# Optimization experiments

Hardware: AMD Instinct MI355X
Metric: run time of the kernel (lower is better)

The kernel has to match this reference:

```python
import jax, jax.numpy as jnp
import numpy as np

N_POINTS, D_EMBED, N_CLUSTERS = 131072, 512, 512
ALPHA = 100.0   # softmax sharpness (python scalar in original forward)
LAMBD = 0.1     # loss weight (init arg in original)


def setup_inputs() -> dict:
    key = jax.random.key(0)
    k1, k2 = jax.random.split(key)
    embeddings = jax.random.normal(k1, (N_POINTS, D_EMBED), dtype=jnp.float32)
    centroids = jax.random.normal(k2, (N_CLUSTERS, D_EMBED), dtype=jnp.float32)
    alpha = jnp.float32(ALPHA)
    lambd = jnp.float32(LAMBD)
    return {"embeddings": embeddings, "centroids": centroids, "alpha": alpha, "lambd": lambd}


def reference(embeddings, centroids, alpha, lambd):
    # Squared euclidean distance to every centroid, computed via GEMM expansion
    # instead of the original per-centroid python loop:
    #   dist[n, k] = ||x_n||^2 - 2 x_n . c_k + ||c_k||^2
    x2 = jnp.sum(embeddings * embeddings, axis=1, keepdims=True)   # [N, 1]
    c2 = jnp.sum(centroids * centroids, axis=1)                    # [K]
    dist = x2 - 2.0 * (embeddings @ centroids.T) + c2[None, :]     # [N, K]
    # Original: exp(-alpha*(d - min_k d)) / sum == stable softmax of -alpha*d over k.
    w = jax.nn.softmax(-alpha * dist, axis=1)                      # [N, K]
    # lambd * mean over points of softmax-weighted distance sum over clusters.
    return lambd * jnp.mean(jnp.sum(dist * w, axis=1))
```

## Files before the change

kernel.cpp:

```cpp
#include <hip/hip_runtime.h>
#include <stdint.h>

#define NPTS   131072
#define DEMB   512
#define NCL    512
#define BM     64
#define NCHUNK 8
#define NTHREADS 256
#define NBLK   (NPTS / BM)

typedef __attribute__((ext_vector_type(4))) float f32x4;

#define WS_CB   0u
#define WS_C2   262144u
#define WS_PART 264192u

static __device__ __forceinline__ float sq4(f32x4 v) {
  return v[0] * v[0] + v[1] * v[1] + v[2] * v[2] + v[3] * v[3];
}

#define LOAD_B8F(DST, BASE)                                                    \
  asm volatile("global_load_dwordx2 %0, %8, off\n\t"                           \
               "global_load_dwordx2 %1, %8, off offset:512\n\t"                \
               "global_load_dwordx2 %2, %8, off offset:1024\n\t"               \
               "global_load_dwordx2 %3, %8, off offset:1536\n\t"               \
               "global_load_dwordx2 %4, %8, off offset:2048\n\t"               \
               "global_load_dwordx2 %5, %8, off offset:2560\n\t"               \
               "global_load_dwordx2 %6, %8, off offset:3072\n\t"               \
               "global_load_dwordx2 %7, %8, off offset:3584"                   \
               : "=&v"((DST)[0]), "=&v"((DST)[1]), "=&v"((DST)[2]),            \
                 "=&v"((DST)[3]), "=&v"((DST)[4]), "=&v"((DST)[5]),            \
                 "=&v"((DST)[6]), "=&v"((DST)[7])                              \
               : "v"(BASE)                                                     \
               : "memory")

#define LOAD_E4(D, P)                                                          \
  asm volatile("global_load_dwordx4 %0, %4, off\n\t"                           \
               "global_load_dwordx4 %1, %4, off offset:16\n\t"                 \
               "global_load_dwordx4 %2, %4, off offset:32\n\t"                 \
               "global_load_dwordx4 %3, %4, off offset:48"                     \
               : "=&v"(D[0]), "=&v"(D[1]), "=&v"(D[2]), "=&v"(D[3])            \
               : "v"(P)                                                        \
               : "memory")

#define WAITV(N)                                                               \
  do {                                                                         \
    asm volatile("s_waitcnt vmcnt(" #N ")" ::: "memory");                      \
    __builtin_amdgcn_sched_barrier(0);                                         \
  } while (0)

#define BAR()                                                                  \
  do {                                                                         \
    asm volatile("s_waitcnt lgkmcnt(0)" ::: "memory");                         \
    __builtin_amdgcn_s_barrier();                                              \
  } while (0)

__global__ __launch_bounds__(128) void prep_kernel(const float* __restrict__ cent,
                                                   uint8_t* __restrict__ ws) {
  const int k = blockIdx.x;
  const int t = threadIdx.x;
  float4 v = ((const float4*)(cent + (size_t)k * DEMB))[t];
  float sq = v.x * v.x + v.y * v.y + v.z * v.z + v.w * v.w;
#pragma unroll
  for (int m = 1; m < 64; m <<= 1) sq += __shfl_xor(sq, m, 64);
  __shared__ float red[2];
  if ((t & 63) == 0) red[t >> 6] = sq;
  __syncthreads();
  if (t == 0) ((float*)(ws + WS_C2))[k] = red[0] + red[1];

  int p = __builtin_amdgcn_cvt_pk_fp8_f32(v.x, v.y, 0, false);
  p = __builtin_amdgcn_cvt_pk_fp8_f32(v.z, v.w, p, true);

  const int d = t * 4;
  const int ch = d >> 6;
  const int dd = d & 63;
  const int kk = dd >> 5;
  const int lhi = (dd >> 3) & 3;
  const int w = k >> 7;
  const int n = (k >> 4) & 7;
  const int l15 = k & 15;
  const int lane = lhi * 16 + l15;
  const uint32_t off = (uint32_t)(ch * 32768 + w * 8192 + kk * 4096 + n * 512 +
                                  lane * 8 + (dd & 7));
  *(uint32_t*)(ws + WS_CB + off) = (uint32_t)p;
}

__global__ __launch_bounds__(NTHREADS, 2) void main_kernel(
    const float* __restrict__ emb, const uint8_t* __restrict__ ws,
    const float* __restrict__ alphap) {
  __shared__ uint8_t Ab[2][4096];
  __shared__ float redmin[256];
  __shared__ float redse[256];
  __shared__ float redsge[256];
  __shared__ float gmin[64];
  __shared__ float x2s[64];

  const int t = threadIdx.x;
  const int w = t >> 6;
  const int l = t & 63;
  const int l15 = l & 15;
  const int lhi = l >> 4;
  const int bid = blockIdx.x;
  const size_t row0 = (size_t)bid * BM;

  float* partials = (float*)(ws + WS_PART);

  f32x4 acc[4][8];
#pragma unroll
  for (int m = 0; m < 4; ++m)
#pragma unroll
    for (int n = 0; n < 8; ++n) acc[m][n] = (f32x4){0.f, 0.f, 0.f, 0.f};

  const int r = t >> 2;
  const int q = t & 3;
  const float* xge = emb + (row0 + r) * DEMB + q * 16;
  uint32_t xoff[2];
#pragma unroll
  for (int j = 0; j < 2; ++j)
    xoff[j] = (uint32_t)r * 64u + (uint32_t)(((2 * q + j) ^ (r & 7)) << 3);

  float x2a = 0.f;

  const uint8_t* fbw = ws + WS_CB + (uint32_t)w * 8192u + (uint32_t)l * 8u;

  long bA[16], bB[16];
  f32x4 ev0[4], ev1[4];

#define STAGE_FROM(EV, DSTBUF)                                                 \
  do {                                                                         \
    uint8_t* _an = (DSTBUF);                                                   \
    _Pragma("unroll")                                                          \
    for (int j = 0; j < 2; ++j) {                                              \
      f32x4 a = EV[2 * j], b = EV[2 * j + 1];                                  \
      x2a += sq4(a) + sq4(b);                                                  \
      uint2 u;                                                                 \
      int p0 = __builtin_amdgcn_cvt_pk_fp8_f32(a[0], a[1], 0, false);          \
      p0 = __builtin_amdgcn_cvt_pk_fp8_f32(a[2], a[3], p0, true);              \
      int p1 = __builtin_amdgcn_cvt_pk_fp8_f32(b[0], b[1], 0, false);          \
      p1 = __builtin_amdgcn_cvt_pk_fp8_f32(b[2], b[3], p1, true);              \
      u.x = (uint32_t)p0;                                                      \
      u.y = (uint32_t)p1;                                                      \
      *(uint2*)(_an + xoff[j]) = u;                                            \
    }                                                                          \
  } while (0)

  LOAD_E4(ev0, xge);
  LOAD_E4(ev1, xge + 64);
  LOAD_B8F(&bA[0], fbw);
  LOAD_B8F(&bA[8], fbw + 4096);
  WAITV(20);
  STAGE_FROM(ev0, &Ab[0][0]);
  BAR();

#define CHUNK_BODY(CH, BCUR, BNEXT, EVN, EVS, VN)                              \
  {                                                                            \
    if ((CH) + 2 < NCHUNK)                                                     \
      LOAD_E4(EVN, xge + ((CH) + 2) * 64);                                     \
    if ((CH) + 1 < NCHUNK) {                                                   \
      const uint8_t* nb = fbw + (uint32_t)((CH) + 1) * 32768u;                 \
      LOAD_B8F(&BNEXT[0], nb);                                                 \
      LOAD_B8F(&BNEXT[8], nb + 4096);                                          \
    }                                                                          \
    const uint8_t* xb = &Ab[(CH) & 1][0];                                      \
    WAITV(VN);                                                                 \
    __builtin_amdgcn_s_setprio(1);                                             \
    _Pragma("unroll")                                                          \
    for (int kk = 0; kk < 2; ++kk) {                                           \
      const uint32_t swz = (uint32_t)(((kk * 4 + lhi) ^ (l15 & 7)) << 3);      \
      long af[4];                                                              \
      _Pragma("unroll")                                                        \
      for (int m = 0; m < 4; ++m)                                              \
        af[m] = *(const long*)(xb + (uint32_t)(m * 16 + l15) * 64u + swz);     \
      _Pragma("unroll")                                                        \
      for (int m = 0; m < 4; ++m)                                              \
        _Pragma("unroll")                                                      \
        for (int n = 0; n < 8; ++n)                                            \
          acc[m][n] = __builtin_amdgcn_mfma_f32_16x16x32_fp8_fp8(              \
              af[m], BCUR[kk * 8 + n], acc[m][n], 0, 0, 0);                    \
    }                                                                          \
    __builtin_amdgcn_s_setprio(0);                                             \
    if ((CH) + 1 < NCHUNK)                                                     \
      STAGE_FROM(EVS, &Ab[((CH) + 1) & 1][0]);                                 \
    BAR();                                                                     \
  }

  CHUNK_BODY(0, bA, bB, ev0, ev1, 20)
  CHUNK_BODY(1, bB, bA, ev1, ev0, 20)
  CHUNK_BODY(2, bA, bB, ev0, ev1, 20)
  CHUNK_BODY(3, bB, bA, ev1, ev0, 20)
  CHUNK_BODY(4, bA, bB, ev0, ev1, 20)
  CHUNK_BODY(5, bB, bA, ev1, ev0, 20)
  CHUNK_BODY(6, bA, bB, ev0, ev1, 16)
  CHUNK_BODY(7, bB, bA, ev1, ev0, 0)
#undef CHUNK_BODY
#undef STAGE_FROM

  const float alpha = alphap[0];
  float c2r[8];
  {
    const float* c2p = (const float*)(ws + WS_C2) + w * 128 + l15;
    asm volatile("global_load_dword %0, %8, off\n\t"
                 "global_load_dword %1, %8, off offset:64\n\t"
                 "global_load_dword %2, %8, off offset:128\n\t"
                 "global_load_dword %3, %8, off offset:192\n\t"
                 "global_load_dword %4, %8, off offset:256\n\t"
                 "global_load_dword %5, %8, off offset:320\n\t"
                 "global_load_dword %6, %8, off offset:384\n\t"
                 "global_load_dword %7, %8, off offset:448"
                 : "=&v"(c2r[0]), "=&v"(c2r[1]), "=&v"(c2r[2]), "=&v"(c2r[3]),
                   "=&v"(c2r[4]), "=&v"(c2r[5]), "=&v"(c2r[6]), "=&v"(c2r[7])
                 : "v"(c2p)
                 : "memory");
    asm volatile("s_waitcnt vmcnt(0)" ::: "memory");
    __builtin_amdgcn_sched_barrier(0);
  }

  x2a += __shfl_xor(x2a, 1, 64);
  x2a += __shfl_xor(x2a, 2, 64);
  if ((l & 3) == 0) x2s[r] = x2a;

  float rmin[4][4];
#pragma unroll
  for (int m = 0; m < 4; ++m)
#pragma unroll
    for (int i = 0; i < 4; ++i) {
      float mn = c2r[0] - 2.f * acc[m][0][i];
#pragma unroll
      for (int n = 1; n < 8; ++n) mn = fminf(mn, c2r[n] - 2.f * acc[m][n][i]);
      rmin[m][i] = mn;
    }
#pragma unroll
  for (int msk = 1; msk < 16; msk <<= 1)
#pragma unroll
    for (int m = 0; m < 4; ++m)
#pragma unroll
      for (int i = 0; i < 4; ++i)
        rmin[m][i] = fminf(rmin[m][i], __shfl_xor(rmin[m][i], msk, 64));
  if (l15 == 0) {
#pragma unroll
    for (int m = 0; m < 4; ++m)
#pragma unroll
      for (int i = 0; i < 4; ++i)
        redmin[w * 64 + m * 16 + lhi * 4 + i] = rmin[m][i];
  }
  __syncthreads();
  if (t < 64) {
    float mn = redmin[t];
#pragma unroll
    for (int w2 = 1; w2 < 4; ++w2) mn = fminf(mn, redmin[w2 * 64 + t]);
    gmin[t] = mn;
  }
  __syncthreads();
#pragma unroll
  for (int m = 0; m < 4; ++m) {
#pragma unroll
    for (int i = 0; i < 4; ++i) {
      const int row = m * 16 + lhi * 4 + i;
      const float M = gmin[row];
      float se = 0.f, sge = 0.f;
#pragma unroll
      for (int n = 0; n < 8; ++n) {
        const float g = c2r[n] - 2.f * acc[m][n][i];
        const float gm = g - M;
        const float e = __expf(-alpha * gm);
        se += e;
        sge += gm * e;
      }
#pragma unroll
      for (int msk = 1; msk < 16; msk <<= 1) {
        se += __shfl_xor(se, msk, 64);
        sge += __shfl_xor(sge, msk, 64);
      }
      if (l15 == 0) {
        redse[w * 64 + row] = se;
        redsge[w * 64 + row] = sge;
      }
    }
  }
  __syncthreads();
  if (t < 64) {
    float Se = 0.f, Sge = 0.f;
#pragma unroll
    for (int w2 = 0; w2 < 4; ++w2) {
      Se += redse[w2 * 64 + t];
      Sge += redsge[w2 * 64 + t];
    }
    float v = gmin[t] + Sge / Se + x2s[t];
#pragma unroll
    for (int msk = 1; msk < 64; msk <<= 1) v += __shfl_xor(v, msk, 64);
    if (t == 0) partials[bid] = v;
  }
}

__global__ __launch_bounds__(256) void final_kernel(const uint8_t* __restrict__ ws,
                                                    const float* __restrict__ lambdp,
                                                    float* __restrict__ out) {
  const float* partials = (const float*)(ws + WS_PART);
  const int t = threadIdx.x;
  float s = 0.f;
  for (int i = t; i < NBLK; i += 256) s += partials[i];
#pragma unroll
  for (int msk = 1; msk < 64; msk <<= 1) s += __shfl_xor(s, msk, 64);
  __shared__ float red[4];
  if ((t & 63) == 0) red[t >> 6] = s;
  __syncthreads();
  if (t == 0)
    out[0] = lambdp[0] * (red[0] + red[1] + red[2] + red[3]) * (1.0f / (float)NPTS);
}

extern "C" void kernel_launch(void* const* d_in, const int* in_sizes, int n_in,
                              void* d_out, int out_size, void* d_ws, size_t ws_size,
                              hipStream_t stream) {
  const float* emb = (const float*)d_in[0];
  const float* cent = (const float*)d_in[1];
  const float* alphap = (const float*)d_in[2];
  const float* lambdp = (const float*)d_in[3];
  float* out = (float*)d_out;
  uint8_t* ws = (uint8_t*)d_ws;

  prep_kernel<<<NCL, 128, 0, stream>>>(cent, ws);
  main_kernel<<<NBLK, NTHREADS, 0, stream>>>(emb, ws, alphap);
  final_kernel<<<1, 256, 0, stream>>>(ws, lambdp, out);
}
```

Measured before the change: 99.61 us.

## Switch to scaled 16x16x128 FP8 MFMA with 128-wide K chunks and repacked centroids

Replaces the 16x16x32 FP8 MFMA with the gfx950 scaled 16x16x128 f8f6f4 MFMA using unit scales. It repacks the FP8 centroid buffer for 128-wide K bodies and doubles the LDS staging buffer. The loop drops from 8 to 4 iterations. Fewer, wider MFMA instructions are meant to raise matrix throughput and cut instruction and barrier overhead. The centroid prefetch is now a single buffer that is only issued after the compute and a full vmcnt(0) wait, so load latency is less well hidden.

```diff
diff --git a/kernel.cpp b/kernel.cpp
--- a/kernel.cpp
+++ b/kernel.cpp
@@ -5,11 +5,13 @@
 #define DEMB   512
 #define NCL    512
 #define BM     64
-#define NCHUNK 8
+#define NBODY  4
 #define NTHREADS 256
 #define NBLK   (NPTS / BM)
 
 typedef __attribute__((ext_vector_type(4))) float f32x4;
+typedef __attribute__((ext_vector_type(4))) int   i32x4;
+typedef __attribute__((ext_vector_type(8))) int   i32x8;
 
 #define WS_CB   0u
 #define WS_C2   262144u
@@ -19,27 +21,26 @@
   return v[0] * v[0] + v[1] * v[1] + v[2] * v[2] + v[3] * v[3];
 }
 
-#define LOAD_B8F(DST, BASE)                                                    \
-  asm volatile("global_load_dwordx2 %0, %8, off\n\t"                           \
-               "global_load_dwordx2 %1, %8, off offset:512\n\t"                \
-               "global_load_dwordx2 %2, %8, off offset:1024\n\t"               \
-               "global_load_dwordx2 %3, %8, off offset:1536\n\t"               \
-               "global_load_dwordx2 %4, %8, off offset:2048\n\t"               \
-               "global_load_dwordx2 %5, %8, off offset:2560\n\t"               \
-               "global_load_dwordx2 %6, %8, off offset:3072\n\t"               \
-               "global_load_dwordx2 %7, %8, off offset:3584"                   \
-               : "=&v"((DST)[0]), "=&v"((DST)[1]), "=&v"((DST)[2]),            \
-                 "=&v"((DST)[3]), "=&v"((DST)[4]), "=&v"((DST)[5]),            \
-                 "=&v"((DST)[6]), "=&v"((DST)[7])                              \
+#define LOAD_B4Q(D0, D1, D2, D3, BASE)                                         \
+  asm volatile("global_load_dwordx4 %0, %4, off\n\t"                           \
+               "global_load_dwordx4 %1, %4, off offset:16\n\t"                 \
+               "global_load_dwordx4 %2, %4, off offset:2048\n\t"               \
+               "global_load_dwordx4 %3, %4, off offset:2064"                   \
+               : "=&v"(D0), "=&v"(D1), "=&v"(D2), "=&v"(D3)                    \
                : "v"(BASE)                                                     \
                : "memory")
 
-#define LOAD_E4(D, P)                                                          \
-  asm volatile("global_load_dwordx4 %0, %4, off\n\t"                           \
-               "global_load_dwordx4 %1, %4, off offset:16\n\t"                 \
-               "global_load_dwordx4 %2, %4, off offset:32\n\t"                 \
-               "global_load_dwordx4 %3, %4, off offset:48"                     \
-               : "=&v"(D[0]), "=&v"(D[1]), "=&v"(D[2]), "=&v"(D[3])            \
+#define LOAD_E8(D, P)                                                          \
+  asm volatile("global_load_dwordx4 %0, %8, off\n\t"                           \
+               "global_load_dwordx4 %1, %8, off offset:16\n\t"                 \
+               "global_load_dwordx4 %2, %8, off offset:32\n\t"                 \
+               "global_load_dwordx4 %3, %8, off offset:48\n\t"                 \
+               "global_load_dwordx4 %4, %8, off offset:64\n\t"                 \
+               "global_load_dwordx4 %5, %8, off offset:80\n\t"                 \
+               "global_load_dwordx4 %6, %8, off offset:96\n\t"                 \
+               "global_load_dwordx4 %7, %8, off offset:112"                    \
+               : "=&v"(D[0]), "=&v"(D[1]), "=&v"(D[2]), "=&v"(D[3]),           \
+                 "=&v"(D[4]), "=&v"(D[5]), "=&v"(D[6]), "=&v"(D[7])            \
                : "v"(P)                                                        \
                : "memory")
 
@@ -72,23 +73,23 @@
   p = __builtin_amdgcn_cvt_pk_fp8_f32(v.z, v.w, p, true);
 
   const int d = t * 4;
-  const int ch = d >> 6;
-  const int dd = d & 63;
-  const int kk = dd >> 5;
-  const int lhi = (dd >> 3) & 3;
+  const int body = d >> 7;
+  const int kin = d & 127;
+  const int lq = kin >> 5;
+  const int e = kin & 31;
   const int w = k >> 7;
   const int n = (k >> 4) & 7;
   const int l15 = k & 15;
-  const int lane = lhi * 16 + l15;
-  const uint32_t off = (uint32_t)(ch * 32768 + w * 8192 + kk * 4096 + n * 512 +
-                                  lane * 8 + (dd & 7));
+  const int lane = lq * 16 + l15;
+  const uint32_t off = (uint32_t)(body * 65536 + w * 16384 + n * 2048 +
+                                  lane * 32 + e);
   *(uint32_t*)(ws + WS_CB + off) = (uint32_t)p;
 }
 
 __global__ __launch_bounds__(NTHREADS, 2) void main_kernel(
     const float* __restrict__ emb, const uint8_t* __restrict__ ws,
     const float* __restrict__ alphap) {
-  __shared__ uint8_t Ab[2][4096];
+  __shared__ uint8_t Ab[2][8192];
   __shared__ float redmin[256];
   __shared__ float redse[256];
   __shared__ float redsge[256];
@@ -104,6 +105,7 @@
   const size_t row0 = (size_t)bid * BM;
 
   float* partials = (float*)(ws + WS_PART);
+  const int SC1 = 0x7f7f7f7f;
 
   f32x4 acc[4][8];
 #pragma unroll
@@ -113,86 +115,91 @@
 
   const int r = t >> 2;
   const int q = t & 3;
-  const float* xge = emb + (row0 + r) * DEMB + q * 16;
+  const float* xge = emb + (row0 + r) * DEMB + q * 32;
   uint32_t xoff[2];
 #pragma unroll
   for (int j = 0; j < 2; ++j)
-    xoff[j] = (uint32_t)r * 64u + (uint32_t)(((2 * q + j) ^ (r & 7)) << 3);
+    xoff[j] = (uint32_t)r * 128u + (uint32_t)(((2 * q + j) ^ (r & 7)) << 4);
 
   float x2a = 0.f;
 
-  const uint8_t* fbw = ws + WS_CB + (uint32_t)w * 8192u + (uint32_t)l * 8u;
-
-  long bA[16], bB[16];
-  f32x4 ev0[4], ev1[4];
-
-#define STAGE_FROM(EV, DSTBUF)                                                 \
+  const uint8_t* fbw = ws + WS_CB + (uint32_t)w * 16384u + (uint32_t)l * 32u;
+
+  const uint32_t s0off = (uint32_t)(((2 * lhi) ^ (l15 & 7)) << 4);
+  const uint32_t s1off = (uint32_t)(((2 * lhi + 1) ^ (l15 & 7)) << 4);
+
+  i32x4 bf[16];
+  f32x4 ev[8];
+
+#define STAGE_FROM(DSTBUF)                                                     \
   do {                                                                         \
     uint8_t* _an = (DSTBUF);                                                   \
     _Pragma("unroll")                                                          \
     for (int j = 0; j < 2; ++j) {                                              \
-      f32x4 a = EV[2 * j], b = EV[2 * j + 1];                                  \
-      x2a += sq4(a) + sq4(b);                                                  \
-      uint2 u;                                                                 \
-      int p0 = __builtin_amdgcn_cvt_pk_fp8_f32(a[0], a[1], 0, false);          \
-      p0 = __builtin_amdgcn_cvt_pk_fp8_f32(a[2], a[3], p0, true);              \
-      int p1 = __builtin_amdgcn_cvt_pk_fp8_f32(b[0], b[1], 0, false);          \
-      p1 = __builtin_amdgcn_cvt_pk_fp8_f32(b[2], b[3], p1, true);              \
-      u.x = (uint32_t)p0;                                                      \
-      u.y = (uint32_t)p1;                                                      \
-      *(uint2*)(_an + xoff[j]) = u;                                            \
+      i32x4 u;                                                                 \
+      _Pragma("unroll")                                                        \
+      for (int i2 = 0; i2 < 4; ++i2) {                                         \
+        f32x4 vv = ev[j * 4 + i2];                                             \
+        x2a += sq4(vv);                                                        \
+        int p0 = __builtin_amdgcn_cvt_pk_fp8_f32(vv[0], vv[1], 0, false);      \
+        p0 = __builtin_amdgcn_cvt_pk_fp8_f32(vv[2], vv[3], p0, true);          \
+        u[i2] = p0;                                                            \
+      }                                                                        \
+      *(i32x4*)(_an + xoff[j]) = u;                                            \
     }                                                                          \
   } while (0)
 
-  LOAD_E4(ev0, xge);
-  LOAD_E4(ev1, xge + 64);
-  LOAD_B8F(&bA[0], fbw);
-  LOAD_B8F(&bA[8], fbw + 4096);
-  WAITV(20);
-  STAGE_FROM(ev0, &Ab[0][0]);
+#define LOAD_B16(BASE)                                                         \
+  do {                                                                         \
+    const uint8_t* _bb = (BASE);                                               \
+    LOAD_B4Q(bf[0], bf[1], bf[2], bf[3], _bb);                                 \
+    LOAD_B4Q(bf[4], bf[5], bf[6], bf[7], _bb + 4096);                          \
+    LOAD_B4Q(bf[8], bf[9], bf[10], bf[11], _bb + 8192);                        \
+    LOAD_B4Q(bf[12], bf[13], bf[14], bf[15], _bb + 12288);                     \
+  } while (0)
+
+  LOAD_E8(ev, xge);
+  LOAD_B16(fbw);
+  WAITV(16);
+  STAGE_FROM(&Ab[0][0]);
   BAR();
 
-#define CHUNK_BODY(CH, BCUR, BNEXT, EVN, EVS, VN)                              \
+#define CHUNK_BODY(B, VNPRE)                                                   \
   {                                                                            \
-    if ((CH) + 2 < NCHUNK)                                                     \
-      LOAD_E4(EVN, xge + ((CH) + 2) * 64);                                     \
-    if ((CH) + 1 < NCHUNK) {                                                   \
-      const uint8_t* nb = fbw + (uint32_t)((CH) + 1) * 32768u;                 \
-      LOAD_B8F(&BNEXT[0], nb);                                                 \
-      LOAD_B8F(&BNEXT[8], nb + 4096);                                          \
-    }                                                                          \
-    const uint8_t* xb = &Ab[(CH) & 1][0];                                      \
-    WAITV(VN);                                                                 \
+    if ((B) + 1 < NBODY)                                                       \
+      LOAD_E8(ev, xge + ((B) + 1) * 128);                                      \
+    const uint8_t* xb = &Ab[(B) & 1][0];                                       \
+    WAITV(VNPRE);                                                              \
     __builtin_amdgcn_s_setprio(1);                                             \
     _Pragma("unroll")                                                          \
-    for (int kk = 0; kk < 2; ++kk) {                                           \
-      const uint32_t swz = (uint32_t)(((kk * 4 + lhi) ^ (l15 & 7)) << 3);      \
-      long af[4];                                                              \
+    for (int m = 0; m < 4; ++m) {                                              \
+      const uint32_t rb = (uint32_t)(m * 16 + l15) * 128u;                     \
+      i32x4 lo = *(const i32x4*)(xb + rb + s0off);                             \
+      i32x4 hi = *(const i32x4*)(xb + rb + s1off);                             \
+      i32x8 a8 = __builtin_shufflevector(lo, hi, 0, 1, 2, 3, 4, 5, 6, 7);      \
       _Pragma("unroll")                                                        \
-      for (int m = 0; m < 4; ++m)                                              \
-        af[m] = *(const long*)(xb + (uint32_t)(m * 16 + l15) * 64u + swz);     \
-      _Pragma("unroll")                                                        \
-      for (int m = 0; m < 4; ++m)                                              \
-        _Pragma("unroll")                                                      \
-        for (int n = 0; n < 8; ++n)                                            \
-          acc[m][n] = __builtin_amdgcn_mfma_f32_16x16x32_fp8_fp8(              \
-              af[m], BCUR[kk * 8 + n], acc[m][n], 0, 0, 0);                    \
+      for (int n = 0; n < 8; ++n) {                                            \
+        i32x8 b8 = __builtin_shufflevector(bf[2 * n], bf[2 * n + 1],           \
+                                           0, 1, 2, 3, 4, 5, 6, 7);            \
+        acc[m][n] = __builtin_amdgcn_mfma_scale_f32_16x16x128_f8f6f4(          \
+            a8, b8, acc[m][n], 0, 0, 0, SC1, 0, SC1);                          \
+      }                                                                        \
     }                                                                          \
     __builtin_amdgcn_s_setprio(0);                                             \
-    if ((CH) + 1 < NCHUNK)                                                     \
-      STAGE_FROM(EVS, &Ab[((CH) + 1) & 1][0]);                                 \
+    if ((B) + 1 < NBODY) {                                                     \
+      WAITV(0);                                                                \
+      STAGE_FROM(&Ab[((B) + 1) & 1][0]);                                       \
+      LOAD_B16(fbw + (uint32_t)((B) + 1) * 65536u);                            \
+    }                                                                          \
     BAR();                                                                     \
   }
 
-  CHUNK_BODY(0, bA, bB, ev0, ev1, 20)
-  CHUNK_BODY(1, bB, bA, ev1, ev0, 20)
-  CHUNK_BODY(2, bA, bB, ev0, ev1, 20)
-  CHUNK_BODY(3, bB, bA, ev1, ev0, 20)
-  CHUNK_BODY(4, bA, bB, ev0, ev1, 20)
-  CHUNK_BODY(5, bB, bA, ev1, ev0, 20)
-  CHUNK_BODY(6, bA, bB, ev0, ev1, 16)
-  CHUNK_BODY(7, bB, bA, ev1, ev0, 0)
+  CHUNK_BODY(0, 8)
+  CHUNK_BODY(1, 8)
+  CHUNK_BODY(2, 8)
+  CHUNK_BODY(3, 0)
 #undef CHUNK_BODY
+#undef LOAD_B16
 #undef STAGE_FROM
 
   const float alpha = alphap[0];
```

Result: slower. 157.5 us (+58.1%).
